# Kernel tuning notes

Measured on AMD Instinct MI355X. Metric: run time of the kernel, lower is better.

## Reference

```python
import jax, jax.numpy as jnp
import numpy as np

B, K, L, D = 64, 64, 128, 128  # batch, top_k, max_length, embedding_dimension
H = 2 * D                      # MLP input size (context || gathered entity)
N_HIDDEN = 6                   # Linear(H,H) layers with Tanh (dropout is eval no-op)


def setup_inputs() -> dict:
    key = jax.random.key(0)
    k0, k1, k2 = jax.random.split(key, 3)
    context = jax.random.normal(k0, (B, K, 2, L, D), dtype=jnp.float32)
    Ws = jax.random.normal(k1, (N_HIDDEN, H, H), dtype=jnp.float32) * 0.05
    bs = jnp.zeros((N_HIDDEN, H), dtype=jnp.float32)
    W_out = jax.random.normal(k2, (H,), dtype=jnp.float32) * 0.05
    b_out = jnp.zeros((), dtype=jnp.float32)
    return {"context": context, "Ws": Ws, "bs": bs, "W_out": W_out, "b_out": b_out}


def reference(context, Ws, bs, W_out, b_out):
    ctx = context[:, :, 0]  # [B,K,L,D]
    ent = context[:, :, 1]  # [B,K,L,D]
    cn = jnp.linalg.norm(ctx, axis=-1, keepdims=True)  # [B,K,L,1]
    en = jnp.linalg.norm(ent, axis=-1, keepdims=True)  # [B,K,L,1]
    # cosine-similarity matrix between context rows and entity rows
    sim = jnp.einsum("bkld,bkmd->bklm", ctx, ent) / (cn * jnp.swapaxes(en, -1, -2))
    ctx_n = ctx / cn
    ent_n = ent / en
    idx = jnp.argmax(sim, axis=-1)  # [B,K,L] top-1 entity row per context row
    gathered = jnp.take_along_axis(
        ent_n, jnp.broadcast_to(idx[..., None], ent_n.shape), axis=2
    )  # [B,K,L,D]
    # stack(...,-2) then flatten(start_dim=-2) == concat along feature dim
    x = jnp.concatenate([ctx_n, gathered], axis=-1)  # [B,K,L,2D]
    for i in range(N_HIDDEN):
        x = jnp.tanh(x @ Ws[i].T + bs[i])
    out = x @ W_out + b_out  # [B,K,L]
    return jnp.sum(out, axis=-1)  # [B,K] (sum over L then squeeze)
```

## Files before the change

kernel.cpp:

```cpp
#include <hip/hip_runtime.h>

#define HID4(r,c4) ((r)*64 + ((((c4) ^ ((r)&15))) << 2))
#define XIDX(r,c)  ((r)*256 + (((((c)>>3) ^ ((r)&7))) << 3) + ((c)&7))

typedef _Float16 half_t;
typedef __attribute__((ext_vector_type(8))) _Float16 f16x8;
typedef __attribute__((ext_vector_type(4))) _Float16 f16x4;
typedef __attribute__((ext_vector_type(4))) float f32x4;

__device__ __forceinline__ float tanh_fast(float x){
    float e = __expf(2.0f * x);
    return 1.0f - 2.0f / (e + 1.0f);
}

__device__ __forceinline__ f16x8 cvt8(float4 a, float4 b){
    f16x8 r;
    r[0]=(half_t)a.x; r[1]=(half_t)a.y; r[2]=(half_t)a.z; r[3]=(half_t)a.w;
    r[4]=(half_t)b.x; r[5]=(half_t)b.y; r[6]=(half_t)b.z; r[7]=(half_t)b.w;
    return r;
}

__global__ __launch_bounds__(256, 2)
void fused_mlp_som(const float* __restrict__ ctx_in,
                   const float* __restrict__ Ws,
                   const float* __restrict__ bs,
                   const float* __restrict__ Wout,
                   const float* __restrict__ bout,
                   float* __restrict__ out)
{
    extern __shared__ char smem[];
    float* S0     = (float*)smem;
    float* S1     = S0 + 128*64;
    float* inv_cn = S1 + 128*64;
    float* inv_en = inv_cn + 128;
    int*   idxm   = (int*)(inv_en + 128);
    float* redbuf = (float*)(idxm + 128);
    half_t* xf    = (half_t*)smem;

    const int tid  = threadIdx.x;
    const int lane = tid & 63;
    const int bk   = blockIdx.x;

    const float*  gctx = ctx_in + (size_t)bk * 32768;
    const float*  gent = gctx + 16384;
    const float4* gc4  = (const float4*)gctx;
    const float4* ge4  = (const float4*)gent;

    const int hf = tid & 1;
    const int nr = tid >> 1;
    float ns = 0.f, nt = 0.f;

    const int ti = tid >> 5;
    const int tj = tid & 31;
    const int l0 = ti * 16;
    float acc[16][4];
    #pragma unroll
    for (int i = 0; i < 16; ++i)
        #pragma unroll
        for (int j = 0; j < 4; ++j) acc[i][j] = 0.f;

    #pragma unroll 1
    for (int h = 0; h < 2; ++h){
        if (h) __syncthreads();
        #pragma unroll
        for (int it = 0; it < 8; ++it){
            int fi = tid + 256*it;
            int r  = fi >> 4;
            int c4 = fi & 15;
            *(float4*)&S0[HID4(r,c4)] = gc4[r*32 + 16*h + c4];
            *(float4*)&S1[HID4(r,c4)] = ge4[r*32 + 16*h + c4];
        }
        __syncthreads();
        if (hf == h){
            #pragma unroll
            for (int u = 0; u < 16; ++u){
                float4 v = *(const float4*)&S0[HID4(nr, u)];
                ns = fmaf(v.x, v.x, ns); ns = fmaf(v.y, v.y, ns);
                ns = fmaf(v.z, v.z, ns); ns = fmaf(v.w, v.w, ns);
                float4 w = *(const float4*)&S1[HID4(nr, u)];
                nt = fmaf(w.x, w.x, nt); nt = fmaf(w.y, w.y, nt);
                nt = fmaf(w.z, w.z, nt); nt = fmaf(w.w, w.w, nt);
            }
        }
        for (int kk = 0; kk < 16; ++kk){
            float4 e0 = *(const float4*)&S1[HID4(tj     , kk)];
            float4 e1 = *(const float4*)&S1[HID4(tj + 32, kk)];
            float4 e2 = *(const float4*)&S1[HID4(tj + 64, kk)];
            float4 e3 = *(const float4*)&S1[HID4(tj + 96, kk)];
            #pragma unroll
            for (int i = 0; i < 16; ++i){
                float4 a = *(const float4*)&S0[HID4(l0+i, kk)];
                acc[i][0] = fmaf(a.x,e0.x,acc[i][0]); acc[i][0] = fmaf(a.y,e0.y,acc[i][0]);
                acc[i][0] = fmaf(a.z,e0.z,acc[i][0]); acc[i][0] = fmaf(a.w,e0.w,acc[i][0]);
                acc[i][1] = fmaf(a.x,e1.x,acc[i][1]); acc[i][1] = fmaf(a.y,e1.y,acc[i][1]);
                acc[i][1] = fmaf(a.z,e1.z,acc[i][1]); acc[i][1] = fmaf(a.w,e1.w,acc[i][1]);
                acc[i][2] = fmaf(a.x,e2.x,acc[i][2]); acc[i][2] = fmaf(a.y,e2.y,acc[i][2]);
                acc[i][2] = fmaf(a.z,e2.z,acc[i][2]); acc[i][2] = fmaf(a.w,e2.w,acc[i][2]);
                acc[i][3] = fmaf(a.x,e3.x,acc[i][3]); acc[i][3] = fmaf(a.y,e3.y,acc[i][3]);
                acc[i][3] = fmaf(a.z,e3.z,acc[i][3]); acc[i][3] = fmaf(a.w,e3.w,acc[i][3]);
            }
        }
    }

    ns += __shfl_xor(ns, 1);
    nt += __shfl_xor(nt, 1);
    if (hf == 0){
        inv_cn[nr] = 1.0f / sqrtf(ns);
        inv_en[nr] = 1.0f / sqrtf(nt);
    }
    __syncthreads();

    #pragma unroll
    for (int i = 0; i < 16; ++i){
        float best = -1e38f; int bi = 0;
        #pragma unroll
        for (int j = 0; j < 4; ++j){
            int m = tj + 32*j;
            float v = acc[i][j] * inv_en[m];
            if (v > best || (v == best && m < bi)){ best = v; bi = m; }
        }
        #pragma unroll
        for (int s = 1; s < 32; s <<= 1){
            float ov = __shfl_xor(best, s);
            int   oi = __shfl_xor(bi,   s);
            if (ov > best || (ov == best && oi < bi)){ best = ov; bi = oi; }
        }
        if (tj == 0) idxm[l0 + i] = bi;
    }
    __syncthreads();

    {
        const int l   = tid >> 1;
        const int sel = tid & 1;
        const float4* src;
        float sc;
        int col0;
        if (sel == 0){ src = (const float4*)(gctx + l*128);          sc = inv_cn[l];  col0 = 0;   }
        else         { int mi = idxm[l]; src = (const float4*)(gent + mi*128); sc = inv_en[mi]; col0 = 128; }
        #pragma unroll
        for (int u = 0; u < 32; ++u){
            float4 v = src[u];
            f16x4 hv;
            hv[0] = (half_t)(v.x * sc); hv[1] = (half_t)(v.y * sc);
            hv[2] = (half_t)(v.z * sc); hv[3] = (half_t)(v.w * sc);
            int c = col0 + 4*u;
            *(f16x4*)&xf[l*256 + ((((c>>3) ^ (l&7))) << 3) + (c&7)] = hv;
        }
    }
    __syncthreads();

    const int wv    = tid >> 6;
    const int lan15 = lane & 15;
    const int lq    = lane >> 4;
    const int kb    = 8*lq;
    const int ncb   = 64*wv;
    const int aBase = lan15*256;

    #pragma unroll 1
    for (int layer = 0; layer < 6; ++layer){
        const float* WsL = Ws + layer*65536;

        f32x4 mac[8][4];
        #pragma unroll
        for (int mt = 0; mt < 8; ++mt)
            #pragma unroll
            for (int nf = 0; nf < 4; ++nf)
                mac[mt][nf] = (f32x4){0.f,0.f,0.f,0.f};

        #pragma unroll 1
        for (int ks = 0; ks < 8; ++ks){
            const int aoff = (((4*ks + lq) ^ (lan15 & 7)) << 3);
            f16x8 b[4];
            #pragma unroll
            for (int nf = 0; nf < 4; ++nf){
                const int bn = (ncb + 16*nf + lan15)*256 + 32*ks + kb;
                float4 qa = *(const float4*)&WsL[bn];
                float4 qb = *(const float4*)&WsL[bn + 4];
                b[nf] = cvt8(qa, qb);
            }
            {
                f16x8 a[4];
                #pragma unroll
                for (int mt = 0; mt < 4; ++mt)
                    a[mt] = *(const f16x8*)&xf[aBase + mt*4096 + aoff];
                #pragma unroll
                for (int mt = 0; mt < 4; ++mt)
                    #pragma unroll
                    for (int nf = 0; nf < 4; ++nf)
                        mac[mt][nf] = __builtin_amdgcn_mfma_f32_16x16x32_f16(a[mt], b[nf], mac[mt][nf], 0,0,0);
            }
            {
                f16x8 a[4];
                #pragma unroll
                for (int mt = 0; mt < 4; ++mt)
                    a[mt] = *(const f16x8*)&xf[aBase + (mt+4)*4096 + aoff];
                #pragma unroll
                for (int mt = 0; mt < 4; ++mt)
                    #pragma unroll
                    for (int nf = 0; nf < 4; ++nf)
                        mac[mt+4][nf] = __builtin_amdgcn_mfma_f32_16x16x32_f16(a[mt], b[nf], mac[mt+4][nf], 0,0,0);
            }
        }
        __syncthreads();

        if (layer < 5){
            float bias[4];
            #pragma unroll
            for (int nf = 0; nf < 4; ++nf) bias[nf] = bs[layer*256 + ncb + 16*nf + lan15];
            #pragma unroll
            for (int mt = 0; mt < 8; ++mt){
                #pragma unroll
                for (int nf = 0; nf < 4; ++nf){
                    const int n = ncb + 16*nf + lan15;
                    #pragma unroll
                    for (int r = 0; r < 4; ++r){
                        int row = 16*mt + 4*lq + r;
                        xf[XIDX(row, n)] = (half_t)tanh_fast(mac[mt][nf][r] + bias[nf]);
                    }
                }
            }
            __syncthreads();
        } else {
            float bias[4], w[4];
            #pragma unroll
            for (int nf = 0; nf < 4; ++nf){
                const int n = ncb + 16*nf + lan15;
                bias[nf] = bs[5*256 + n];
                w[nf]    = Wout[n];
            }
            float part = 0.f;
            #pragma unroll
            for (int mt = 0; mt < 8; ++mt)
                #pragma unroll
                for (int nf = 0; nf < 4; ++nf)
                    #pragma unroll
                    for (int r = 0; r < 4; ++r)
                        part = fmaf(tanh_fast(mac[mt][nf][r] + bias[nf]), w[nf], part);
            #pragma unroll
            for (int s = 1; s < 64; s <<= 1) part += __shfl_xor(part, s);
            if (lane == 0) redbuf[wv] = part;
            __syncthreads();
            if (tid == 0){
                float s = redbuf[0] + redbuf[1] + redbuf[2] + redbuf[3];
                out[bk] = s + 128.0f * bout[0];
            }
        }
    }
}

extern "C" void kernel_launch(void* const* d_in, const int* in_sizes, int n_in,
                              void* d_out, int out_size, void* d_ws, size_t ws_size,
                              hipStream_t stream)
{
    (void)in_sizes; (void)n_in; (void)out_size; (void)d_ws; (void)ws_size;
    const float* ctx  = (const float*)d_in[0];
    const float* Ws   = (const float*)d_in[1];
    const float* bs   = (const float*)d_in[2];
    const float* Wout = (const float*)d_in[3];
    const float* bout = (const float*)d_in[4];
    float* out = (float*)d_out;

    const int smem_bytes = 128*64*4*2 + 128*4 + 128*4 + 128*4 + 4*4;
    hipFuncSetAttribute(reinterpret_cast<const void*>(fused_mlp_som),
                        hipFuncAttributeMaxDynamicSharedMemorySize, smem_bytes);
    fused_mlp_som<<<dim3(4096), dim3(256), smem_bytes, stream>>>(ctx, Ws, bs, Wout, bout, out);
}
```

Before: 1.535 ms.

## Double block size to 512 threads, halving per-thread work in sim and MLP

Launches 512 threads per block instead of 256 and splits every phase across twice as many threads. The similarity GEMM does 8 rows per thread, norm computation is split between context and entity threads, and the MLP gives each wave 32 output columns instead of 64. The goal is fewer registers per thread and more waves in flight to hide global weight loads and LDS latency. In exchange, each wave now re-reads the A fragments from LDS for half the MFMAs, and the per-block register budget (launch bounds 512,4) may force spills or limit occupancy.

```diff
diff --git a/kernel.cpp b/kernel.cpp
--- a/kernel.cpp
+++ b/kernel.cpp
@@ -5,7 +5,6 @@
 
 typedef _Float16 half_t;
 typedef __attribute__((ext_vector_type(8))) _Float16 f16x8;
-typedef __attribute__((ext_vector_type(4))) _Float16 f16x4;
 typedef __attribute__((ext_vector_type(4))) float f32x4;
 
 __device__ __forceinline__ float tanh_fast(float x){
@@ -20,7 +19,7 @@
     return r;
 }
 
-__global__ __launch_bounds__(256, 2)
+__global__ __launch_bounds__(512, 4)
 void fused_mlp_som(const float* __restrict__ ctx_in,
                    const float* __restrict__ Ws,
                    const float* __restrict__ bs,
@@ -46,16 +45,17 @@
     const float4* gc4  = (const float4*)gctx;
     const float4* ge4  = (const float4*)gent;
 
-    const int hf = tid & 1;
-    const int nr = tid >> 1;
-    float ns = 0.f, nt = 0.f;
+    const int isEnt = tid >> 8;
+    const int hf    = tid & 1;
+    const int nr    = (tid >> 1) & 127;
+    float ns = 0.f;
 
     const int ti = tid >> 5;
     const int tj = tid & 31;
-    const int l0 = ti * 16;
-    float acc[16][4];
+    const int l0 = ti * 8;
+    float acc[8][4];
     #pragma unroll
-    for (int i = 0; i < 16; ++i)
+    for (int i = 0; i < 8; ++i)
         #pragma unroll
         for (int j = 0; j < 4; ++j) acc[i][j] = 0.f;
 
@@ -63,8 +63,8 @@
     for (int h = 0; h < 2; ++h){
         if (h) __syncthreads();
         #pragma unroll
-        for (int it = 0; it < 8; ++it){
-            int fi = tid + 256*it;
+        for (int it = 0; it < 4; ++it){
+            int fi = tid + 512*it;
             int r  = fi >> 4;
             int c4 = fi & 15;
             *(float4*)&S0[HID4(r,c4)] = gc4[r*32 + 16*h + c4];
@@ -72,14 +72,12 @@
         }
         __syncthreads();
         if (hf == h){
+            const float* T = isEnt ? S1 : S0;
             #pragma unroll
             for (int u = 0; u < 16; ++u){
-                float4 v = *(const float4*)&S0[HID4(nr, u)];
+                float4 v = *(const float4*)&T[HID4(nr, u)];
                 ns = fmaf(v.x, v.x, ns); ns = fmaf(v.y, v.y, ns);
                 ns = fmaf(v.z, v.z, ns); ns = fmaf(v.w, v.w, ns);
-                float4 w = *(const float4*)&S1[HID4(nr, u)];
-                nt = fmaf(w.x, w.x, nt); nt = fmaf(w.y, w.y, nt);
-                nt = fmaf(w.z, w.z, nt); nt = fmaf(w.w, w.w, nt);
             }
         }
         for (int kk = 0; kk < 16; ++kk){
@@ -88,7 +86,7 @@
             float4 e2 = *(const float4*)&S1[HID4(tj + 64, kk)];
             float4 e3 = *(const float4*)&S1[HID4(tj + 96, kk)];
             #pragma unroll
-            for (int i = 0; i < 16; ++i){
+            for (int i = 0; i < 8; ++i){
                 float4 a = *(const float4*)&S0[HID4(l0+i, kk)];
                 acc[i][0] = fmaf(a.x,e0.x,acc[i][0]); acc[i][0] = fmaf(a.y,e0.y,acc[i][0]);
                 acc[i][0] = fmaf(a.z,e0.z,acc[i][0]); acc[i][0] = fmaf(a.w,e0.w,acc[i][0]);
@@ -103,15 +101,14 @@
     }
 
     ns += __shfl_xor(ns, 1);
-    nt += __shfl_xor(nt, 1);
     if (hf == 0){
-        inv_cn[nr] = 1.0f / sqrtf(ns);
-        inv_en[nr] = 1.0f / sqrtf(nt);
+        float inv = 1.0f / sqrtf(ns);
+        if (isEnt) inv_en[nr] = inv; else inv_cn[nr] = inv;
     }
     __syncthreads();
 
     #pragma unroll
-    for (int i = 0; i < 16; ++i){
+    for (int i = 0; i < 8; ++i){
         float best = -1e38f; int bi = 0;
         #pragma unroll
         for (int j = 0; j < 4; ++j){
@@ -130,21 +127,22 @@
     __syncthreads();
 
     {
-        const int l   = tid >> 1;
-        const int sel = tid & 1;
+        const int l = tid >> 2;
+        const int q = tid & 3;
         const float4* src;
         float sc;
-        int col0;
-        if (sel == 0){ src = (const float4*)(gctx + l*128);          sc = inv_cn[l];  col0 = 0;   }
-        else         { int mi = idxm[l]; src = (const float4*)(gent + mi*128); sc = inv_en[mi]; col0 = 128; }
-        #pragma unroll
-        for (int u = 0; u < 32; ++u){
-            float4 v = src[u];
-            f16x4 hv;
-            hv[0] = (half_t)(v.x * sc); hv[1] = (half_t)(v.y * sc);
-            hv[2] = (half_t)(v.z * sc); hv[3] = (half_t)(v.w * sc);
-            int c = col0 + 4*u;
-            *(f16x4*)&xf[l*256 + ((((c>>3) ^ (l&7))) << 3) + (c&7)] = hv;
+        int c0;
+        if (q < 2){ src = (const float4*)(gctx + l*128 + 64*q);  sc = inv_cn[l]; c0 = 64*q; }
+        else { int mi = idxm[l]; src = (const float4*)(gent + mi*128 + 64*(q-2)); sc = inv_en[mi]; c0 = 128 + 64*(q-2); }
+        #pragma unroll
+        for (int u = 0; u < 8; ++u){
+            float4 va = src[2*u];
+            float4 vb = src[2*u+1];
+            f16x8 hv;
+            hv[0]=(half_t)(va.x*sc); hv[1]=(half_t)(va.y*sc); hv[2]=(half_t)(va.z*sc); hv[3]=(half_t)(va.w*sc);
+            hv[4]=(half_t)(vb.x*sc); hv[5]=(half_t)(vb.y*sc); hv[6]=(half_t)(vb.z*sc); hv[7]=(half_t)(vb.w*sc);
+            int c = c0 + 8*u;
+            *(f16x8*)&xf[l*256 + ((((c>>3) ^ (l&7))) << 3)] = hv;
         }
     }
     __syncthreads();
@@ -152,31 +150,36 @@
     const int wv    = tid >> 6;
     const int lan15 = lane & 15;
     const int lq    = lane >> 4;
+    const int n0    = 32*wv + lan15;
+    const int n1    = n0 + 16;
+    const int bno0  = n0 * 256;
+    const int bno1  = n1 * 256;
     const int kb    = 8*lq;
-    const int ncb   = 64*wv;
     const int aBase = lan15*256;
 
     #pragma unroll 1
     for (int layer = 0; layer < 6; ++layer){
         const float* WsL = Ws + layer*65536;
 
-        f32x4 mac[8][4];
-        #pragma unroll
-        for (int mt = 0; mt < 8; ++mt)
-            #pragma unroll
-            for (int nf = 0; nf < 4; ++nf)
-                mac[mt][nf] = (f32x4){0.f,0.f,0.f,0.f};
+        f32x4 mac[8][2];
+        #pragma unroll
+        for (int mt = 0; mt < 8; ++mt){
+            mac[mt][0] = (f32x4){0.f,0.f,0.f,0.f};
+            mac[mt][1] = (f32x4){0.f,0.f,0.f,0.f};
+        }
 
         #pragma unroll 1
         for (int ks = 0; ks < 8; ++ks){
             const int aoff = (((4*ks + lq) ^ (lan15 & 7)) << 3);
-            f16x8 b[4];
-            #pragma unroll
-            for (int nf = 0; nf < 4; ++nf){
-                const int bn = (ncb + 16*nf + lan15)*256 + 32*ks + kb;
-                float4 qa = *(const float4*)&WsL[bn];
-                float4 qb = *(const float4*)&WsL[bn + 4];
-                b[nf] = cvt8(qa, qb);
+            f16x8 b0, b1;
+            {
+                const int kk = 32*ks + kb;
+                float4 qa = *(const float4*)&WsL[bno0 + kk];
+                float4 qb = *(const float4*)&WsL[bno0 + kk + 4];
+                b0 = cvt8(qa, qb);
+                float4 qc = *(const float4*)&WsL[bno1 + kk];
+                float4 qd = *(const float4*)&WsL[bno1 + kk + 4];
+                b1 = cvt8(qc, qd);
             }
             {
                 f16x8 a[4];
@@ -184,10 +187,10 @@
                 for (int mt = 0; mt < 4; ++mt)
                     a[mt] = *(const f16x8*)&xf[aBase + mt*4096 + aoff];
                 #pragma unroll
-                for (int mt = 0; mt < 4; ++mt)
-                    #pragma unroll
-                    for (int nf = 0; nf < 4; ++nf)
-                        mac[mt][nf] = __builtin_amdgcn_mfma_f32_16x16x32_f16(a[mt], b[nf], mac[mt][nf], 0,0,0);
+                for (int mt = 0; mt < 4; ++mt){
+                    mac[mt][0] = __builtin_amdgcn_mfma_f32_16x16x32_f16(a[mt], b0, mac[mt][0], 0,0,0);
+                    mac[mt][1] = __builtin_amdgcn_mfma_f32_16x16x32_f16(a[mt], b1, mac[mt][1], 0,0,0);
+                }
             }
             {
                 f16x8 a[4];
@@ -195,53 +198,49 @@
                 for (int mt = 0; mt < 4; ++mt)
                     a[mt] = *(const f16x8*)&xf[aBase + (mt+4)*4096 + aoff];
                 #pragma unroll
-                for (int mt = 0; mt < 4; ++mt)
-                    #pragma unroll
-                    for (int nf = 0; nf < 4; ++nf)
-                        mac[mt+4][nf] = __builtin_amdgcn_mfma_f32_16x16x32_f16(a[mt], b[nf], mac[mt+4][nf], 0,0,0);
+                for (int mt = 0; mt < 4; ++mt){
+                    mac[mt+4][0] = __builtin_amdgcn_mfma_f32_16x16x32_f16(a[mt], b0, mac[mt+4][0], 0,0,0);
+                    mac[mt+4][1] = __builtin_amdgcn_mfma_f32_16x16x32_f16(a[mt], b1, mac[mt+4][1], 0,0,0);
+                }
             }
         }
         __syncthreads();
 
         if (layer < 5){
-            float bias[4];
-            #pragma unroll
-            for (int nf = 0; nf < 4; ++nf) bias[nf] = bs[layer*256 + ncb + 16*nf + lan15];
+            float bias0 = bs[layer*256 + n0];
+            float bias1 = bs[layer*256 + n1];
             #pragma unroll
             for (int mt = 0; mt < 8; ++mt){
                 #pragma unroll
-                for (int nf = 0; nf < 4; ++nf){
-                    const int n = ncb + 16*nf + lan15;
-                    #pragma unroll
-                    for (int r = 0; r < 4; ++r){
-                        int row = 16*mt + 4*lq + r;
-                        xf[XIDX(row, n)] = (half_t)tanh_fast(mac[mt][nf][r] + bias[nf]);
-                    }
+                for (int r = 0; r < 4; ++r){
+                    int row = 16*mt + 4*lq + r;
+                    xf[XIDX(row, n0)] = (half_t)tanh_fast(mac[mt][0][r] + bias0);
+                    xf[XIDX(row, n1)] = (half_t)tanh_fast(mac[mt][1][r] + bias1);
                 }
             }
             __syncthreads();
         } else {
-            float bias[4], w[4];
-            #pragma unroll
-            for (int nf = 0; nf < 4; ++nf){
-                const int n = ncb + 16*nf + lan15;
-                bias[nf] = bs[5*256 + n];
-                w[nf]    = Wout[n];
-            }
+            float bias0 = bs[5*256 + n0];
+            float bias1 = bs[5*256 + n1];
+            float w0 = Wout[n0];
+            float w1 = Wout[n1];
             float part = 0.f;
             #pragma unroll
-            for (int mt = 0; mt < 8; ++mt)
-                #pragma unroll
-                for (int nf = 0; nf < 4; ++nf)
-                    #pragma unroll
-                    for (int r = 0; r < 4; ++r)
-                        part = fmaf(tanh_fast(mac[mt][nf][r] + bias[nf]), w[nf], part);
+            for (int mt = 0; mt < 8; ++mt){
+                #pragma unroll
+                for (int r = 0; r < 4; ++r){
+                    part = fmaf(tanh_fast(mac[mt][0][r] + bias0), w0, part);
+                    part = fmaf(tanh_fast(mac[mt][1][r] + bias1), w1, part);
+                }
+            }
             #pragma unroll
             for (int s = 1; s < 64; s <<= 1) part += __shfl_xor(part, s);
             if (lane == 0) redbuf[wv] = part;
             __syncthreads();
             if (tid == 0){
-                float s = redbuf[0] + redbuf[1] + redbuf[2] + redbuf[3];
+                float s = 0.f;
+                #pragma unroll
+                for (int i = 0; i < 8; ++i) s += redbuf[i];
                 out[bk] = s + 128.0f * bout[0];
             }
         }
@@ -260,8 +259,8 @@
     const float* bout = (const float*)d_in[4];
     float* out = (float*)d_out;
 
-    const int smem_bytes = 128*64*4*2 + 128*4 + 128*4 + 128*4 + 4*4;
+    const int smem_bytes = 128*64*4*2 + 128*4 + 128*4 + 128*4 + 8*4;
     hipFuncSetAttribute(reinterpret_cast<const void*>(fused_mlp_som),
                         hipFuncAttributeMaxDynamicSharedMemorySize, smem_bytes);
-    fused_mlp_som<<<dim3(4096), dim3(256), smem_bytes, stream>>>(ctx, Ws, bs, Wout, bout, out);
-}
+    fused_mlp_som<<<dim3(4096), dim3(512), smem_bytes, stream>>>(ctx, Ws, bs, Wout, bout, out);
+}
```

Measured after the change: 1.382 ms. 1.11x faster.
